# Optimization experiments

Measured on AMD Instinct MI355X. Metric: run time of the kernel, lower is better.

## Reference

```python
import jax, jax.numpy as jnp
import numpy as np

B, T, F, U, OUT_STEPS = 128, 256, 64, 1024, 32
D_HID = 32  # dense head hidden width


def lstm_step(h, c, x, W, R, b):
    # Keras gate order: i, f, g (cell candidate), o
    z = x @ W + h @ R + b  # [B, 4U]
    i, f, g, o = jnp.split(z, 4, axis=-1)
    c_new = jax.nn.sigmoid(f) * c + jax.nn.sigmoid(i) * jnp.tanh(g)
    h_new = jax.nn.sigmoid(o) * jnp.tanh(c_new)
    return h_new, c_new


def setup_inputs() -> dict:
    key = jax.random.key(0)
    ks = jax.random.split(key, 16)
    s = 0.05  # small init scale to keep gates unsaturated
    return {
        "inputs": jax.random.normal(ks[0], (B, T, F), jnp.float32),
        # encoder LSTM layer (input dim F)
        "Wl": jax.random.normal(ks[1], (F, 4 * U), jnp.float32) * s,
        "Rl": jax.random.normal(ks[2], (U, 4 * U), jnp.float32) * s,
        "bl": jnp.zeros((4 * U,), jnp.float32),
        "Wc": jax.random.normal(ks[3], (F, 4 * U), jnp.float32) * s,
        "Rc": jax.random.normal(ks[4], (U, 4 * U), jnp.float32) * s,
        "bc": jnp.zeros((4 * U,), jnp.float32),
        # rnn_cell (an LSTMCell; input dim = units, fed lstm_cell output)
        "Wr": jax.random.normal(ks[5], (U, 4 * U), jnp.float32) * s,
        "Rr": jax.random.normal(ks[6], (U, 4 * U), jnp.float32) * s,
        "br": jnp.zeros((4 * U,), jnp.float32),
        # dense head: Dense(32, relu) -> Dense(num_features)
        "W1": jax.random.normal(ks[7], (U, D_HID), jnp.float32) * s,
        "b1": jnp.zeros((D_HID,), jnp.float32),
        "W2": jax.random.normal(ks[8], (D_HID, F), jnp.float32) * s,
        "b2": jnp.zeros((F,), jnp.float32),
    }


def reference(inputs, Wl, Rl, bl, Wc, Rc, bc, Wr, Rr, br, W1, b1, W2, b2):
    b = inputs.shape[0]
    h0 = jnp.zeros((b, U), inputs.dtype)
    c0 = jnp.zeros((b, U), inputs.dtype)

    def enc_step(carry, x_t):
        h, c = carry
        h, c = lstm_step(h, c, x_t, Wl, Rl, bl)
        return (h, c), None

    # encoder LSTM over time (scan over T, batch-parallel)
    (h, c), _ = jax.lax.scan(enc_step, (h0, c0), jnp.swapaxes(inputs, 0, 1))

    dense = lambda x: jax.nn.relu(x @ W1 + b1) @ W2 + b2

    pred0 = dense(h)  # [B, F]
    # state_rnn initialized from encoder final state (same values, evolves separately)
    init = (pred0, h, c, h, c)

    def ar_step(carry, _):
        pred, hl, cl, hr, cr = carry
        hl, cl = lstm_step(hl, cl, pred, Wc, Rc, bc)
        hr, cr = lstm_step(hr, cr, hl, Wr, Rr, br)
        pred = dense(hr)
        return (pred, hl, cl, hr, cr), pred

    _, preds = jax.lax.scan(ar_step, init, None, length=OUT_STEPS - 1)
    preds = jnp.concatenate([pred0[None], preds], axis=0)  # [OUT, B, F]
    return jnp.transpose(preds, (1, 0, 2))  # [B, OUT, F]
```

## Files before the change

### kernel.cpp

```cpp
#include <hip/hip_runtime.h>

typedef unsigned short u16;
typedef unsigned int u32;
typedef unsigned long long u64;
typedef short v8s __attribute__((ext_vector_type(8)));
typedef int v4i __attribute__((ext_vector_type(4)));
typedef float f32x4 __attribute__((ext_vector_type(4)));

#define NB 128
#define NU 1024
#define NF 64
#define NT 256
#define NOUT 32
#define NBLK 256
#define XS 72
#define FPAD 32
#define GO_OFF (NBLK * FPAD)
#define ZBS 66

__device__ __forceinline__ u16 f2bf(float f) {
  union { float f; u32 u; } v; v.f = f;
  u32 x = v.u;
  return (u16)((x + 0x7fffu + ((x >> 16) & 1u)) >> 16);
}
__device__ __forceinline__ float bf2f(u16 u) {
  union { u32 u; float f; } v; v.u = ((u32)u) << 16;
  return v.f;
}

__device__ __forceinline__ void cstore32(u32* p, u32 v) {
  __hip_atomic_store(p, v, __ATOMIC_RELAXED, __HIP_MEMORY_SCOPE_AGENT);
}
__device__ __forceinline__ v4i cload128(const void* p) {
  v4i r;
  asm volatile("global_load_dwordx4 %0, %1, off sc0 sc1" : "=v"(r) : "v"(p) : "memory");
  return r;
}

__device__ __forceinline__ void gbar(u32* bar, u32 gen, int grp, int wgn, int tid) {
  asm volatile("s_waitcnt vmcnt(0)" ::: "memory");
  __syncthreads();
  const int bid = grp * 64 + wgn;
  if (tid == 0)
    __hip_atomic_store(&bar[bid * FPAD], gen, __ATOMIC_RELAXED, __HIP_MEMORY_SCOPE_AGENT);
  u32* go = bar + GO_OFF;
  if (wgn == 0) {
    if (tid < 64) {
      const u32* fl = bar + (size_t)(grp * 64 + tid) * FPAD;
      bool ok = false;
      u32 spin = 0;
      for (;;) {
        if (!ok)
          ok = __hip_atomic_load(fl, __ATOMIC_RELAXED, __HIP_MEMORY_SCOPE_AGENT) >= gen;
        if (__all(ok)) break;
        __builtin_amdgcn_s_sleep(2);
        if (++spin > 2000000u) break;
      }
      __hip_atomic_store(&go[(grp * 64 + tid) * FPAD], gen, __ATOMIC_RELAXED,
                         __HIP_MEMORY_SCOPE_AGENT);
    }
  } else if (tid == 0) {
    const u32* fl = go + (size_t)bid * FPAD;
    u32 spin = 0;
    while (__hip_atomic_load(fl, __ATOMIC_RELAXED, __HIP_MEMORY_SCOPE_AGENT) < gen) {
      __builtin_amdgcn_s_sleep(2);
      if (++spin > 2000000u) break;
    }
  }
  __syncthreads();
  asm volatile("" ::: "memory");
}

__global__ void init_bar(u32* bar) {
  int i = blockIdx.x * 256 + threadIdx.x;
  if (i < 2 * NBLK * FPAD) bar[i] = 0;
}

__global__ void pack_weights(const float* __restrict__ top, const float* __restrict__ R,
                             int ktop, int nchunk, u16* __restrict__ dst) {
  int line = blockIdx.x * 256 + threadIdx.x;
  int l = line & 63;
  int rest = line >> 6;
  int s = rest & 1; rest >>= 1;
  int kk = rest % nchunk;
  int t  = rest / nchunk;
  if (t >= 256) return;
  int kbase = kk * 64 + s * 32 + (l >> 4) * 8;
  int col = ((l >> 2) & 3) * 1024 + t * 4 + (l & 3);
  v8s o;
#pragma unroll
  for (int j = 0; j < 8; ++j) {
    int k = kbase + j;
    float v = (k < ktop) ? top[(size_t)k * 4096 + col]
                         : R[(size_t)(k - ktop) * 4096 + col];
    o[j] = (short)f2bf(v);
  }
  *(v8s*)(void*)(dst + (size_t)line * 8) = o;
}

__global__ void pack_w1(const float* __restrict__ W1, u16* __restrict__ dst) {
  int id = blockIdx.x * 256 + threadIdx.x;
  int lane = id & 63;
  int line = id >> 6;
  int res = line >> 6;
  int cl = line & 63;
  int c = cl >> 1, nt = cl & 1;
  int krow = c * 32 + ((lane >> 4) * 8);
  int col = nt * 16 + (lane & 15);
  v8s o;
#pragma unroll
  for (int j = 0; j < 8; ++j) {
    float v = W1[(size_t)(krow + j) * 32 + col];
    u16 hi = f2bf(v);
    o[j] = (short)(res ? f2bf(v - bf2f(hi)) : hi);
  }
  *(v8s*)(void*)(dst + (size_t)id * 8) = o;
}

struct P {
  const float* x;
  const u16 *packE, *packC, *packR, *W1f;
  const float *bl, *bc, *br, *b1, *W2, *b2;
  u16 *hxE0, *hxE1, *hxL0, *hxL1, *hxR0, *hxR1;
  float* out;
  u32* bar;
};

__device__ __forceinline__ v8s ldA(const u16* Asb, int row, int unit) {
  return *(const v8s*)(const void*)(Asb + row * 2048 + ((unit ^ (row & 7)) * 8));
}

__device__ __forceinline__ void stageHX(u16* Asb, int tid, const u16* hx, int dstu) {
  v4i t[16];
#pragma unroll
  for (int i = 0; i < 16; ++i) {
    int q = tid + i * 256;
    t[i] = cload128(hx + (size_t)q * 8);
  }
  asm volatile("s_waitcnt vmcnt(0)" ::: "memory");
#pragma unroll
  for (int i = 0; i < 16; ++i) {
    int q = tid + i * 256;
    int sb = q >> 6, rem = q & 63;
    int r = rem >> 1, c8 = rem & 1;
    int u = (dstu + sb * 2 + c8) ^ (r & 7);
    *(v4i*)(void*)(Asb + r * 2048 + u * 8) = t[i];
  }
}

__device__ __forceinline__ void stageH2X(u16* Asb, int tid,
                                         const u16* hxa, const u16* hxb) {
  v4i a[16], b[16];
#pragma unroll
  for (int i = 0; i < 16; ++i) {
    int q = tid + i * 256;
    a[i] = cload128(hxa + (size_t)q * 8);
  }
#pragma unroll
  for (int i = 0; i < 16; ++i) {
    int q = tid + i * 256;
    b[i] = cload128(hxb + (size_t)q * 8);
  }
  asm volatile("s_waitcnt vmcnt(0)" ::: "memory");
#pragma unroll
  for (int i = 0; i < 16; ++i) {
    int q = tid + i * 256;
    int sb = q >> 6, rem = q & 63;
    int r = rem >> 1, c8 = rem & 1;
    int u = (sb * 2 + c8) ^ (r & 7);
    *(v4i*)(void*)(Asb + r * 2048 + u * 8) = a[i];
  }
#pragma unroll
  for (int i = 0; i < 16; ++i) {
    int q = tid + i * 256;
    int sb = q >> 6, rem = q & 63;
    int r = rem >> 1, c8 = rem & 1;
    int u = (128 + sb * 2 + c8) ^ (r & 7);
    *(v4i*)(void*)(Asb + r * 2048 + u * 8) = b[i];
  }
}

__device__ __forceinline__ void stageX(u16* Xsb, int tid, int m0,
                                       const float* x, int t) {
#pragma unroll
  for (int i = 0; i < 4; ++i) {
    int idx = tid + i * 256;
    int ml = idx >> 5, dw = idx & 31;
    const float* sp = x + ((size_t)(m0 + ml) * NT + t) * NF + dw * 2;
    u32 v = (u32)f2bf(sp[0]) | ((u32)f2bf(sp[1]) << 16);
    *(u32*)(void*)(Xsb + ml * XS + dw * 2) = v;
  }
}

template <int NCH, int XCH>
__device__ __forceinline__ void mfmaSK(f32x4 (&acc)[4][2], const u16* Asb,
                                       const u16* Xsb, const u16* pack,
                                       int linesz, int tile0,
                                       int w, int lane, int quad, int l15) {
  const u16* tb0 = pack + (size_t)(tile0 + 0) * linesz;
  const u16* tb1 = pack + (size_t)(tile0 + 1) * linesz;
  const u16* tb2 = pack + (size_t)(tile0 + 2) * linesz;
  const u16* tb3 = pack + (size_t)(tile0 + 3) * linesz;
  for (int j = w; j < NCH; j += 4) {
    v8s a0, a1;
    if (XCH > 0 && j < XCH) {
      a0 = *(const v8s*)(const void*)(Xsb + l15 * XS + j * 32 + quad * 8);
      a1 = *(const v8s*)(const void*)(Xsb + (16 + l15) * XS + j * 32 + quad * 8);
    } else {
      int u = (j - XCH) * 4 + quad;
      a0 = ldA(Asb, l15, u);
      a1 = ldA(Asb, 16 + l15, u);
    }
    size_t bo = (size_t)(j * 64 + lane) * 8;
    v8s b0 = *(const v8s*)(const void*)(tb0 + bo);
    v8s b1 = *(const v8s*)(const void*)(tb1 + bo);
    v8s b2 = *(const v8s*)(const void*)(tb2 + bo);
    v8s b3 = *(const v8s*)(const void*)(tb3 + bo);
    acc[0][0] = __builtin_amdgcn_mfma_f32_16x16x32_bf16(a0, b0, acc[0][0], 0, 0, 0);
    acc[1][0] = __builtin_amdgcn_mfma_f32_16x16x32_bf16(a0, b1, acc[1][0], 0, 0, 0);
    acc[2][0] = __builtin_amdgcn_mfma_f32_16x16x32_bf16(a0, b2, acc[2][0], 0, 0, 0);
    acc[3][0] = __builtin_amdgcn_mfma_f32_16x16x32_bf16(a0, b3, acc[3][0], 0, 0, 0);
    acc[0][1] = __builtin_amdgcn_mfma_f32_16x16x32_bf16(a1, b0, acc[0][1], 0, 0, 0);
    acc[1][1] = __builtin_amdgcn_mfma_f32_16x16x32_bf16(a1, b1, acc[1][1], 0, 0, 0);
    acc[2][1] = __builtin_amdgcn_mfma_f32_16x16x32_bf16(a1, b2, acc[2][1], 0, 0, 0);
    acc[3][1] = __builtin_amdgcn_mfma_f32_16x16x32_bf16(a1, b3, acc[3][1], 0, 0, 0);
  }
}

__device__ __forceinline__ void gates_store(float* zb, u16* hpk,
                                            int w, int lane, int quad, int l15,
                                            int wgn, int bid,
                                            const f32x4 (&acc)[4][2],
                                            const float* bias,
                                            float cpair[2], u16* hxout, bool czero) {
  __syncthreads();
#pragma unroll
  for (int tt = 0; tt < 4; ++tt)
#pragma unroll
    for (int rt = 0; rt < 2; ++rt)
#pragma unroll
      for (int r = 0; r < 4; ++r)
        zb[(size_t)(w * 32 + rt * 16 + quad * 4 + r) * ZBS + tt * 16 + l15] =
            acc[tt][rt][r];
  __syncthreads();
  const int tblk = wgn * 4 + w;
#pragma unroll
  for (int rep = 0; rep < 2; ++rep) {
    int pp = lane + rep * 64;
    int ml = pp >> 2;
    int cc = pp & 3;
    int col = tblk * 4 + cc;
    float zg[4];
#pragma unroll
    for (int g = 0; g < 4; ++g) {
      int zc = w * 16 + g * 4 + cc;
      float s = zb[(size_t)(0 * 32 + ml) * ZBS + zc] +
                zb[(size_t)(1 * 32 + ml) * ZBS + zc] +
                zb[(size_t)(2 * 32 + ml) * ZBS + zc] +
                zb[(size_t)(3 * 32 + ml) * ZBS + zc];
      zg[g] = s + bias[g * 1024 + col];
    }
    float cold = czero ? 0.f : cpair[rep];
    float si = 1.f / (1.f + __expf(-zg[0]));
    float sf = 1.f / (1.f + __expf(-zg[1]));
    float so = 1.f / (1.f + __expf(-zg[3]));
    float e2g = __expf(2.f * zg[2]);
    float tg  = (e2g - 1.f) / (e2g + 1.f);
    float cn  = sf * cold + si * tg;
    float e2c = __expf(2.f * cn);
    float tc  = (e2c - 1.f) / (e2c + 1.f);
    cpair[rep] = cn;
    hpk[w * 128 + ml * 4 + cc] = f2bf(so * tc);
  }
  __syncthreads();
  {
    int tid = w * 64 + lane;
    int r = tid >> 3, c2 = tid & 7;
    int wsrc = c2 >> 1;
    u32 v = *(const u32*)(const void*)(hpk + wsrc * 128 + r * 4 + (c2 & 1) * 2);
    cstore32((u32*)(void*)(hxout + (size_t)bid * 512) + r * 8 + c2, v);
  }
}

__device__ __forceinline__ void dense_head(const P& p, const u16* Asb, float* d1s,
                                           u16* Xsb, int tid, int w, int lane,
                                           int quad, int l15, int m0, int step,
                                           bool wout) {
  const int rt = w >> 1, ct = w & 1;
  const int arow = rt * 16 + l15;
  const u16* wf = p.W1f;
  f32x4 acc0 = {0.f, 0.f, 0.f, 0.f}, acc1 = acc0;
#pragma unroll
  for (int k = 0; k < 16; ++k) {
    v8s b0 = *(const v8s*)(const void*)(wf + ((size_t)((2 * k) * 2 + ct) * 64 + lane) * 8);
    v8s a0 = ldA(Asb, arow, 128 + (2 * k) * 4 + quad);
    v8s b1 = *(const v8s*)(const void*)(wf + ((size_t)((2 * k + 1) * 2 + ct) * 64 + lane) * 8);
    v8s a1 = ldA(Asb, arow, 128 + (2 * k + 1) * 4 + quad);
    acc0 = __builtin_amdgcn_mfma_f32_16x16x32_bf16(a0, b0, acc0, 0, 0, 0);
    acc1 = __builtin_amdgcn_mfma_f32_16x16x32_bf16(a1, b1, acc1, 0, 0, 0);
  }
#pragma unroll
  for (int k = 0; k < 16; ++k) {
    v8s b0 = *(const v8s*)(const void*)(wf + ((size_t)(64 + (2 * k) * 2 + ct) * 64 + lane) * 8);
    v8s a0 = ldA(Asb, arow, 128 + (2 * k) * 4 + quad);
    v8s b1 = *(const v8s*)(const void*)(wf + ((size_t)(64 + (2 * k + 1) * 2 + ct) * 64 + lane) * 8);
    v8s a1 = ldA(Asb, arow, 128 + (2 * k + 1) * 4 + quad);
    acc0 = __builtin_amdgcn_mfma_f32_16x16x32_bf16(a0, b0, acc0, 0, 0, 0);
    acc1 = __builtin_amdgcn_mfma_f32_16x16x32_bf16(a1, b1, acc1, 0, 0, 0);
  }
  acc0 += acc1;
  const int col = ct * 16 + l15;
  const float b1c = p.b1[col];
#pragma unroll
  for (int r = 0; r < 4; ++r) {
    int row = rt * 16 + quad * 4 + r;
    d1s[row * 33 + col] = fmaxf(acc0[r] + b1c, 0.f);
  }
  __syncthreads();
  const int r = tid >> 3, cb = (tid & 7) * 8;
  float s2[8];
#pragma unroll
  for (int cc = 0; cc < 8; ++cc) s2[cc] = p.b2[cb + cc];
#pragma unroll
  for (int k = 0; k < 32; ++k) {
    float dv = d1s[r * 33 + k];
    f32x4 w20 = *(const f32x4*)(const void*)(p.W2 + k * 64 + cb);
    f32x4 w21 = *(const f32x4*)(const void*)(p.W2 + k * 64 + cb + 4);
    s2[0] += dv * w20[0]; s2[1] += dv * w20[1];
    s2[2] += dv * w20[2]; s2[3] += dv * w20[3];
    s2[4] += dv * w21[0]; s2[5] += dv * w21[1];
    s2[6] += dv * w21[2]; s2[7] += dv * w21[3];
  }
#pragma unroll
  for (int cc = 0; cc < 8; ++cc) Xsb[r * XS + cb + cc] = f2bf(s2[cc]);
  if (wout) {
    float* po = p.out + ((size_t)(m0 + r) * NOUT + step) * NF + cb;
#pragma unroll
    for (int cc = 0; cc < 8; ++cc) po[cc] = s2[cc];
  }
  __syncthreads();
}

__global__ void __launch_bounds__(256, 1) rnn_persist(P p) {
  __shared__ __align__(16) u16 Asb[32 * 2048];
  __shared__ __align__(16) u16 Xsb[32 * XS];
  __shared__ float d1s[32 * 33];
  __shared__ u16 hpack[512];
  float* zb = (float*)(void*)Asb;

  const int tid = threadIdx.x;
  const int bid = blockIdx.x;
  const int wgn = bid & 63;
  const int mg  = bid >> 6;
  const int m0  = mg * 32;
  const int w    = tid >> 6;
  const int lane = tid & 63;
  const int quad = lane >> 4;
  const int l15  = lane & 15;
  const int tile0 = wgn * 4;
  const size_t gsl = (size_t)mg * 64 * 512;

  float cE2[2] = {0.f, 0.f};
  u32 bno = 0;

  stageX(Xsb, tid, m0, p.x, 0);
  for (int t = 0; t < NT; ++t) {
    const u16* hread = ((t & 1) ? p.hxE1 : p.hxE0) + gsl;
    u16* hwrite      = (t & 1) ? p.hxE0 : p.hxE1;
    f32x4 acc[4][2];
#pragma unroll
    for (int a = 0; a < 4; ++a)
#pragma unroll
      for (int b = 0; b < 2; ++b) acc[a][b] = (f32x4){0.f, 0.f, 0.f, 0.f};
    if (t > 0) {
      stageHX(Asb, tid, hread, 0);
      __syncthreads();
      mfmaSK<34, 2>(acc, Asb, Xsb, p.packE, 17408, tile0, w, lane, quad, l15);
    } else {
      __syncthreads();
      mfmaSK<2, 2>(acc, Asb, Xsb, p.packE, 17408, tile0, w, lane, quad, l15);
    }
    gates_store(zb, hpack, w, lane, quad, l15, wgn, bid, acc,
                p.bl, cE2, hwrite, t == 0);
    if (t + 1 < NT) stageX(Xsb, tid, m0, p.x, t + 1);
    ++bno; gbar(p.bar, bno, mg, wgn, tid);
  }

  float cL2[2] = {cE2[0], cE2[1]};
  float cR2[2] = {cE2[0], cE2[1]};
  for (int s = 1; s < NOUT; ++s) {
    const u16* hlr = ((s == 1) ? p.hxE0 : ((s & 1) ? p.hxL1 : p.hxL0)) + gsl;
    const u16* hrd = ((s == 1) ? p.hxE0 : ((s & 1) ? p.hxR1 : p.hxR0)) + gsl;
    u16* hlw = (s & 1) ? p.hxL0 : p.hxL1;
    u16* hrw = (s & 1) ? p.hxR0 : p.hxR1;

    {
      stageH2X(Asb, tid, hlr, hrd);
      __syncthreads();
      dense_head(p, Asb, d1s, Xsb, tid, w, lane, quad, l15, m0, s - 1, wgn == 0);
      f32x4 acc[4][2];
#pragma unroll
      for (int a = 0; a < 4; ++a)
#pragma unroll
        for (int b = 0; b < 2; ++b) acc[a][b] = (f32x4){0.f, 0.f, 0.f, 0.f};
      mfmaSK<34, 2>(acc, Asb, Xsb, p.packC, 17408, tile0, w, lane, quad, l15);
      gates_store(zb, hpack, w, lane, quad, l15, wgn, bid, acc,
                  p.bc, cL2, hlw, false);
    }
    ++bno; gbar(p.bar, bno, mg, wgn, tid);

    {
      stageH2X(Asb, tid, hlw + gsl, hrd);
      __syncthreads();
      f32x4 acc[4][2];
#pragma unroll
      for (int a = 0; a < 4; ++a)
#pragma unroll
        for (int b = 0; b < 2; ++b) acc[a][b] = (f32x4){0.f, 0.f, 0.f, 0.f};
      mfmaSK<64, 0>(acc, Asb, Xsb, p.packR, 32768, tile0, w, lane, quad, l15);
      gates_store(zb, hpack, w, lane, quad, l15, wgn, bid, acc,
                  p.br, cR2, hrw, false);
    }
    ++bno; gbar(p.bar, bno, mg, wgn, tid);
  }

  if (wgn == 0) {
    stageHX(Asb, tid, p.hxR0 + gsl, 128);
    __syncthreads();
    dense_head(p, Asb, d1s, Xsb, tid, w, lane, quad, l15, m0, NOUT - 1, true);
  }
}

extern "C" void kernel_launch(void* const* d_in, const int* in_sizes, int n_in,
                              void* d_out, int out_size, void* d_ws, size_t ws_size,
                              hipStream_t stream) {
  const float* x  = (const float*)d_in[0];
  const float* Wl = (const float*)d_in[1];
  const float* Rl = (const float*)d_in[2];
  const float* bl = (const float*)d_in[3];
  const float* Wc = (const float*)d_in[4];
  const float* Rc = (const float*)d_in[5];
  const float* bc = (const float*)d_in[6];
  const float* Wr = (const float*)d_in[7];
  const float* Rr = (const float*)d_in[8];
  const float* br = (const float*)d_in[9];
  const float* W1 = (const float*)d_in[10];
  const float* b1 = (const float*)d_in[11];
  const float* W2 = (const float*)d_in[12];
  const float* b2 = (const float*)d_in[13];

  char* ws = (char*)d_ws;
  size_t off = 0;
  auto alloc = [&](size_t bytes) -> void* {
    void* r = ws + off;
    off += (bytes + 255) & ~(size_t)255;
    return r;
  };
  const size_t szPackE = (size_t)256 * 17408 * 2;
  const size_t szPackR = (size_t)256 * 32768 * 2;
  const size_t szHx    = (size_t)NBLK * 512 * 2;
  u16* packE = (u16*)alloc(szPackE);
  u16* packC = (u16*)alloc(szPackE);
  u16* packR = (u16*)alloc(szPackR);
  u16* W1f   = (u16*)alloc((size_t)128 * 64 * 8 * 2);
  u16* hxE0 = (u16*)alloc(szHx);
  u16* hxE1 = (u16*)alloc(szHx);
  u16* hxL0 = (u16*)alloc(szHx);
  u16* hxL1 = (u16*)alloc(szHx);
  u16* hxR0 = (u16*)alloc(szHx);
  u16* hxR1 = (u16*)alloc(szHx);
  u32* bar = (u32*)alloc(2 * NBLK * FPAD * 4);

  init_bar<<<dim3(64), dim3(256), 0, stream>>>(bar);
  pack_weights<<<dim3(128 * 17), dim3(256), 0, stream>>>(Wl, Rl, 64, 17, packE);
  pack_weights<<<dim3(128 * 17), dim3(256), 0, stream>>>(Wc, Rc, 64, 17, packC);
  pack_weights<<<dim3(128 * 32), dim3(256), 0, stream>>>(Wr, Rr, 1024, 32, packR);
  pack_w1<<<dim3(32), dim3(256), 0, stream>>>(W1, W1f);

  static P p;
  p.x = x;
  p.packE = packE; p.packC = packC; p.packR = packR; p.W1f = W1f;
  p.bl = bl; p.bc = bc; p.br = br;
  p.b1 = b1; p.W2 = W2; p.b2 = b2;
  p.hxE0 = hxE0; p.hxE1 = hxE1;
  p.hxL0 = hxL0; p.hxL1 = hxL1;
  p.hxR0 = hxR0; p.hxR1 = hxR1;
  p.out = (float*)d_out;
  p.bar = bar;

  rnn_persist<<<dim3(NBLK), dim3(256), 0, stream>>>(p);
}
```

Before: 3.264 ms.

## Replace centralized grid barrier with per-wave slice polling before staging

New measurement: 3.014 ms. 7.7% less time.

```diff
diff --git a/kernel.cpp b/kernel.cpp
--- a/kernel.cpp
+++ b/kernel.cpp
@@ -15,7 +15,6 @@
 #define NBLK 256
 #define XS 72
 #define FPAD 32
-#define GO_OFF (NBLK * FPAD)
 #define ZBS 66
 
 __device__ __forceinline__ u16 f2bf(float f) {
@@ -37,38 +36,25 @@
   return r;
 }
 
-__device__ __forceinline__ void gbar(u32* bar, u32 gen, int grp, int wgn, int tid) {
+__device__ __forceinline__ void publish(u32* bar, u32 gen, int bid, int tid) {
   asm volatile("s_waitcnt vmcnt(0)" ::: "memory");
   __syncthreads();
-  const int bid = grp * 64 + wgn;
   if (tid == 0)
     __hip_atomic_store(&bar[bid * FPAD], gen, __ATOMIC_RELAXED, __HIP_MEMORY_SCOPE_AGENT);
-  u32* go = bar + GO_OFF;
-  if (wgn == 0) {
-    if (tid < 64) {
-      const u32* fl = bar + (size_t)(grp * 64 + tid) * FPAD;
-      bool ok = false;
-      u32 spin = 0;
-      for (;;) {
-        if (!ok)
-          ok = __hip_atomic_load(fl, __ATOMIC_RELAXED, __HIP_MEMORY_SCOPE_AGENT) >= gen;
-        if (__all(ok)) break;
-        __builtin_amdgcn_s_sleep(2);
-        if (++spin > 2000000u) break;
-      }
-      __hip_atomic_store(&go[(grp * 64 + tid) * FPAD], gen, __ATOMIC_RELAXED,
-                         __HIP_MEMORY_SCOPE_AGENT);
-    }
-  } else if (tid == 0) {
-    const u32* fl = go + (size_t)bid * FPAD;
-    u32 spin = 0;
-    while (__hip_atomic_load(fl, __ATOMIC_RELAXED, __HIP_MEMORY_SCOPE_AGENT) < gen) {
-      __builtin_amdgcn_s_sleep(2);
-      if (++spin > 2000000u) break;
-    }
-  }
-  __syncthreads();
-  asm volatile("" ::: "memory");
+}
+
+__device__ __forceinline__ void pollslice(const u32* bar, u32 gen, int grp,
+                                          int w, int lane) {
+  const u32* fl = bar + (size_t)(grp * 64 + w * 16 + (lane & 15)) * FPAD;
+  bool ok = (lane >= 16);
+  u32 spin = 0;
+  for (;;) {
+    if (!ok)
+      ok = __hip_atomic_load(fl, __ATOMIC_RELAXED, __HIP_MEMORY_SCOPE_AGENT) >= gen;
+    if (__all(ok)) break;
+    __builtin_amdgcn_s_sleep(1);
+    if (++spin > 4000000u) break;
+  }
 }
 
 __global__ void init_bar(u32* bar) {
@@ -130,54 +116,61 @@
   return *(const v8s*)(const void*)(Asb + row * 2048 + ((unit ^ (row & 7)) * 8));
 }
 
-__device__ __forceinline__ void stageHX(u16* Asb, int tid, const u16* hx, int dstu) {
+__device__ __forceinline__ void stage_bar1(u16* Asb, const u32* bar, u32 gen,
+                                           int grp, int w, int lane,
+                                           const u16* hx, int dstu) {
+  pollslice(bar, gen, grp, w, lane);
   v4i t[16];
 #pragma unroll
-  for (int i = 0; i < 16; ++i) {
-    int q = tid + i * 256;
-    t[i] = cload128(hx + (size_t)q * 8);
+  for (int j = 0; j < 16; ++j) {
+    int q = (w * 16 + j) * 64 + lane;
+    t[j] = cload128(hx + (size_t)q * 8);
   }
   asm volatile("s_waitcnt vmcnt(0)" ::: "memory");
 #pragma unroll
-  for (int i = 0; i < 16; ++i) {
-    int q = tid + i * 256;
+  for (int j = 0; j < 16; ++j) {
+    int q = (w * 16 + j) * 64 + lane;
     int sb = q >> 6, rem = q & 63;
     int r = rem >> 1, c8 = rem & 1;
     int u = (dstu + sb * 2 + c8) ^ (r & 7);
-    *(v4i*)(void*)(Asb + r * 2048 + u * 8) = t[i];
-  }
-}
-
-__device__ __forceinline__ void stageH2X(u16* Asb, int tid,
-                                         const u16* hxa, const u16* hxb) {
+    *(v4i*)(void*)(Asb + r * 2048 + u * 8) = t[j];
+  }
+  __syncthreads();
+}
+
+__device__ __forceinline__ void stage_bar2(u16* Asb, const u32* bar, u32 gen,
+                                           int grp, int w, int lane,
+                                           const u16* hxa, const u16* hxb) {
+  pollslice(bar, gen, grp, w, lane);
   v4i a[16], b[16];
 #pragma unroll
-  for (int i = 0; i < 16; ++i) {
-    int q = tid + i * 256;
-    a[i] = cload128(hxa + (size_t)q * 8);
-  }
-#pragma unroll
-  for (int i = 0; i < 16; ++i) {
-    int q = tid + i * 256;
-    b[i] = cload128(hxb + (size_t)q * 8);
+  for (int j = 0; j < 16; ++j) {
+    int q = (w * 16 + j) * 64 + lane;
+    a[j] = cload128(hxa + (size_t)q * 8);
+  }
+#pragma unroll
+  for (int j = 0; j < 16; ++j) {
+    int q = (w * 16 + j) * 64 + lane;
+    b[j] = cload128(hxb + (size_t)q * 8);
   }
   asm volatile("s_waitcnt vmcnt(0)" ::: "memory");
 #pragma unroll
-  for (int i = 0; i < 16; ++i) {
-    int q = tid + i * 256;
+  for (int j = 0; j < 16; ++j) {
+    int q = (w * 16 + j) * 64 + lane;
     int sb = q >> 6, rem = q & 63;
     int r = rem >> 1, c8 = rem & 1;
     int u = (sb * 2 + c8) ^ (r & 7);
-    *(v4i*)(void*)(Asb + r * 2048 + u * 8) = a[i];
-  }
-#pragma unroll
-  for (int i = 0; i < 16; ++i) {
-    int q = tid + i * 256;
+    *(v4i*)(void*)(Asb + r * 2048 + u * 8) = a[j];
+  }
+#pragma unroll
+  for (int j = 0; j < 16; ++j) {
+    int q = (w * 16 + j) * 64 + lane;
     int sb = q >> 6, rem = q & 63;
     int r = rem >> 1, c8 = rem & 1;
     int u = (128 + sb * 2 + c8) ^ (r & 7);
-    *(v4i*)(void*)(Asb + r * 2048 + u * 8) = b[i];
-  }
+    *(v4i*)(void*)(Asb + r * 2048 + u * 8) = b[j];
+  }
+  __syncthreads();
 }
 
 __device__ __forceinline__ void stageX(u16* Xsb, int tid, int m0,
@@ -373,8 +366,7 @@
 #pragma unroll
       for (int b = 0; b < 2; ++b) acc[a][b] = (f32x4){0.f, 0.f, 0.f, 0.f};
     if (t > 0) {
-      stageHX(Asb, tid, hread, 0);
-      __syncthreads();
+      stage_bar1(Asb, p.bar, bno, mg, w, lane, hread, 0);
       mfmaSK<34, 2>(acc, Asb, Xsb, p.packE, 17408, tile0, w, lane, quad, l15);
     } else {
       __syncthreads();
@@ -383,7 +375,7 @@
     gates_store(zb, hpack, w, lane, quad, l15, wgn, bid, acc,
                 p.bl, cE2, hwrite, t == 0);
     if (t + 1 < NT) stageX(Xsb, tid, m0, p.x, t + 1);
-    ++bno; gbar(p.bar, bno, mg, wgn, tid);
+    publish(p.bar, ++bno, bid, tid);
   }
 
   float cL2[2] = {cE2[0], cE2[1]};
@@ -395,8 +387,7 @@
     u16* hrw = (s & 1) ? p.hxR0 : p.hxR1;
 
     {
-      stageH2X(Asb, tid, hlr, hrd);
-      __syncthreads();
+      stage_bar2(Asb, p.bar, bno, mg, w, lane, hlr, hrd);
       dense_head(p, Asb, d1s, Xsb, tid, w, lane, quad, l15, m0, s - 1, wgn == 0);
       f32x4 acc[4][2];
 #pragma unroll
@@ -407,11 +398,10 @@
       gates_store(zb, hpack, w, lane, quad, l15, wgn, bid, acc,
                   p.bc, cL2, hlw, false);
     }
-    ++bno; gbar(p.bar, bno, mg, wgn, tid);
+    publish(p.bar, ++bno, bid, tid);
 
     {
-      stageH2X(Asb, tid, hlw + gsl, hrd);
-      __syncthreads();
+      stage_bar2(Asb, p.bar, bno, mg, w, lane, hlw + gsl, hrd);
       f32x4 acc[4][2];
 #pragma unroll
       for (int a = 0; a < 4; ++a)
@@ -421,12 +411,11 @@
       gates_store(zb, hpack, w, lane, quad, l15, wgn, bid, acc,
                   p.br, cR2, hrw, false);
     }
-    ++bno; gbar(p.bar, bno, mg, wgn, tid);
+    publish(p.bar, ++bno, bid, tid);
   }
 
   if (wgn == 0) {
-    stageHX(Asb, tid, p.hxR0 + gsl, 128);
-    __syncthreads();
+    stage_bar1(Asb, p.bar, bno, mg, w, lane, p.hxR0 + gsl, 128);
     dense_head(p, Asb, d1s, Xsb, tid, w, lane, quad, l15, m0, NOUT - 1, true);
   }
 }
```
